# Kernel optimization log

Measured on AMD Instinct MI355X. Metric: run time of the kernel, lower is better.

The kernel has to match this reference:

```python
import jax, jax.numpy as jnp
import numpy as np

B, S, D, H = 2, 2048, 1024, 16
DH = D // H  # 64


def setup_inputs() -> dict:
    key = jax.random.key(0)
    ks = jax.random.split(key, 7)
    scale = 0.02
    return {
        "q": jax.random.normal(ks[0], (B, S, D), dtype=jnp.float32),
        "k": jax.random.normal(ks[1], (B, S, D), dtype=jnp.float32),
        "v": jax.random.normal(ks[2], (B, S, D), dtype=jnp.float32),
        "Wq": jax.random.normal(ks[3], (D, D), dtype=jnp.float32) * scale,
        "Wk": jax.random.normal(ks[4], (D, D), dtype=jnp.float32) * scale,
        "Wv": jax.random.normal(ks[5], (D, D), dtype=jnp.float32) * scale,
        "Wo": jax.random.normal(ks[6], (D, D), dtype=jnp.float32) * scale,
    }


def _split_heads(x):
    # [B, S, D] -> [B, H, S, DH]
    b, s, d = x.shape
    return x.reshape(b, s, H, DH).transpose(0, 2, 1, 3)


def reference(q, k, v, Wq, Wk, Wv, Wo):
    # Linear projections (torch Linear: x @ W.T, bias=False)
    qh = _split_heads(q @ Wq.T)  # [B, H, S, DH]
    kh = _split_heads(k @ Wk.T)
    vh = _split_heads(v @ Wv.T)
    # Scaled dot-product attention (manual, materializes scores as original)
    scores = jnp.einsum("bhqd,bhkd->bhqk", qh, kh) / jnp.sqrt(
        jnp.asarray(DH, dtype=qh.dtype)
    )  # [B, H, S, S]
    attn = jax.nn.softmax(scores, axis=-1)
    out = jnp.einsum("bhqk,bhkd->bhqd", attn, vh)  # [B, H, S, DH]
    # Concat heads: [B, H, S, DH] -> [B, S, D]
    out = out.transpose(0, 2, 1, 3).reshape(q.shape[0], q.shape[1], D)
    return out @ Wo.T
```

## Files before the change

kernel.cpp:

```cpp
#include <hip/hip_runtime.h>
#include <hip/hip_bf16.h>
#include <math.h>

namespace {
constexpr int Hn  = 16;
constexpr int DH  = 64;
constexpr int S   = 2048;
constexpr int D   = 1024;
constexpr int B   = 2;
constexpr int N   = B * S;
}

typedef __attribute__((ext_vector_type(8))) short bf16x8;
typedef __attribute__((ext_vector_type(4))) float f32x4;

#if defined(__has_builtin)
#if __has_builtin(__builtin_amdgcn_exp2f)
#define HAVE_EXP2_BUILTIN 1
#endif
#endif

static __device__ __forceinline__ float exp2_fast(float x) {
#ifdef HAVE_EXP2_BUILTIN
    return __builtin_amdgcn_exp2f(x);
#else
    float r;
    asm("v_exp_f32 %0, %1" : "=v"(r) : "v"(x));
    return r;
#endif
}

static __device__ __forceinline__ ushort bf16rd(float x) {
    unsigned u = __builtin_bit_cast(unsigned, x);
    return (ushort)((u + 0x8000u) >> 16);
}
static __device__ __forceinline__ ushort bf16tr(float x) {
    return (ushort)(__builtin_bit_cast(unsigned, x) >> 16);
}
static __device__ __forceinline__ float bfu2f(ushort h) {
    unsigned u = (unsigned)h << 16;
    return __builtin_bit_cast(float, u);
}
static __device__ __forceinline__ void split1(float a, ushort& h, ushort& l) {
    h = bf16rd(a);
    l = bf16rd(a - bfu2f(h));
}

static __device__ __forceinline__ void gload16(const ushort* g, ushort* l) {
    __builtin_amdgcn_global_load_lds((const unsigned int*)g, (unsigned int*)l, 16, 0, 0);
}

__global__ __launch_bounds__(256) void split_all(
    const float4* __restrict__ q, const float4* __restrict__ k, const float4* __restrict__ v,
    const float4* __restrict__ wq, const float4* __restrict__ wk,
    const float4* __restrict__ wv, const float4* __restrict__ wo,
    ushort4* __restrict__ qh, ushort4* __restrict__ kh, ushort4* __restrict__ vh,
    ushort4* __restrict__ wqh, ushort4* __restrict__ wkh, ushort4* __restrict__ wvh,
    ushort4* __restrict__ woh, ushort4* __restrict__ wol,
    int n4a, int n4w) {
    const int total = 3 * n4a + 4 * n4w;
    const int stride = gridDim.x * 256;
    for (int i = blockIdx.x * 256 + threadIdx.x; i < total; i += stride) {
        if (i < 3 * n4a) {
            const int which = i / n4a;
            const int j = i - which * n4a;
            const float4 val = (which == 0 ? q : which == 1 ? k : v)[j];
            ushort4* ph = which == 0 ? qh : which == 1 ? kh : vh;
            ph[j] = make_ushort4(bf16rd(val.x), bf16rd(val.y), bf16rd(val.z), bf16rd(val.w));
        } else {
            const int t = i - 3 * n4a;
            const int which = t / n4w;
            const int j = t - which * n4w;
            const float4 val = (which == 0 ? wq : which == 1 ? wk : which == 2 ? wv : wo)[j];
            if (which == 3) {
                ushort4 hh, ll;
                split1(val.x, hh.x, ll.x);
                split1(val.y, hh.y, ll.y);
                split1(val.z, hh.z, ll.z);
                split1(val.w, hh.w, ll.w);
                woh[j] = hh;
                wol[j] = ll;
            } else {
                ushort4* ph = which == 0 ? wqh : which == 1 ? wkh : wvh;
                ph[j] = make_ushort4(bf16rd(val.x), bf16rd(val.y), bf16rd(val.z), bf16rd(val.w));
            }
        }
    }
}

__global__ __launch_bounds__(256) void gemm_qkv(
    const ushort* __restrict__ qbf, const ushort* __restrict__ kbf,
    const ushort* __restrict__ vbf,
    const ushort* __restrict__ Wqh, const ushort* __restrict__ Wkh,
    const ushort* __restrict__ Wvh,
    ushort* __restrict__ Qbh, ushort* __restrict__ Kbh,
    ushort* __restrict__ Vtb, float qscale) {
    constexpr int BK = 64;
    constexpr int K = D;
    __shared__ __align__(16) ushort sA[128 * BK];
    __shared__ __align__(16) ushort sB[128 * BK];

    const int tid = threadIdx.x;
    const int which = blockIdx.y >> 3;
    const int m0 = blockIdx.x * 128;
    const int n0 = (blockIdx.y & 7) * 128;

    const ushort* A = which == 0 ? qbf : which == 1 ? kbf : vbf;
    const ushort* W = which == 0 ? Wqh : which == 1 ? Wkh : Wvh;

    const int l  = tid & 63;
    const int w  = tid >> 6;
    const int wm = w >> 1, wn = w & 1;
    const int lm = l & 15, g = l >> 4;

    const int srow = l >> 3;
    const int schunk = (l & 7) ^ srow;
    const ushort* gA = A + (size_t)(m0 + w * 32 + srow) * K + schunk * 8;
    const ushort* gB = W + (size_t)(n0 + w * 32 + srow) * K + schunk * 8;
    ushort* lA = &sA[(w * 32) * BK];
    ushort* lB = &sB[(w * 32) * BK];

    const f32x4 fzero = {0.f, 0.f, 0.f, 0.f};
    f32x4 acc[4][4];
#pragma unroll
    for (int mi = 0; mi < 4; ++mi)
#pragma unroll
        for (int ni = 0; ni < 4; ++ni) acc[mi][ni] = fzero;

    const int rsw = lm & 7;

    for (int s = 0; s < K / BK; ++s) {
        const int k0 = s * BK;
        if (s) __syncthreads();
#pragma unroll
        for (int j = 0; j < 4; ++j) {
            gload16(gA + (size_t)(j * 8) * K + k0, lA + (j * 8) * BK);
            gload16(gB + (size_t)(j * 8) * K + k0, lB + (j * 8) * BK);
        }
        __syncthreads();

#pragma unroll
        for (int kk = 0; kk < 2; ++kk) {
            bf16x8 ah[4], bh[4];
#pragma unroll
            for (int mi = 0; mi < 4; ++mi)
                ah[mi] = *(const bf16x8*)&sA[(wm * 64 + mi * 16 + lm) * BK + (((kk * 4 + g) ^ rsw) * 8)];
#pragma unroll
            for (int ni = 0; ni < 4; ++ni)
                bh[ni] = *(const bf16x8*)&sB[(wn * 64 + ni * 16 + lm) * BK + (((kk * 4 + g) ^ rsw) * 8)];
            __builtin_amdgcn_s_setprio(1);
#pragma unroll
            for (int mi = 0; mi < 4; ++mi)
#pragma unroll
                for (int ni = 0; ni < 4; ++ni)
                    acc[mi][ni] = __builtin_amdgcn_mfma_f32_16x16x32_bf16(
                        ah[mi], bh[ni], acc[mi][ni], 0, 0, 0);
            __builtin_amdgcn_s_setprio(0);
        }
    }

#pragma unroll
    for (int mi = 0; mi < 4; ++mi)
#pragma unroll
        for (int ni = 0; ni < 4; ++ni) {
            const int col = n0 + wn * 64 + ni * 16 + lm;
            const int rbase = m0 + wm * 64 + mi * 16 + g * 4;
            const int hh = col >> 6, dh = col & (DH - 1);
            if (which == 0) {
#pragma unroll
                for (int r = 0; r < 4; ++r) {
                    const int row = rbase + r;
                    const int bb = row >> 11, ss = row & (S - 1);
                    const size_t idx = (((size_t)(bb * Hn + hh)) * S + ss) * DH + dh;
                    Qbh[idx] = bf16rd(acc[mi][ni][r] * qscale);
                }
            } else if (which == 1) {
#pragma unroll
                for (int r = 0; r < 4; ++r) {
                    const int row = rbase + r;
                    const int bb = row >> 11, ss = row & (S - 1);
                    const size_t idx = (((size_t)(bb * Hn + hh)) * S + ss) * DH + dh;
                    Kbh[idx] = bf16rd(acc[mi][ni][r]);
                }
            } else {
                const int bb = rbase >> 11, ss = rbase & (S - 1);
                ushort4 pk;
                pk.x = bf16rd(acc[mi][ni][0]);
                pk.y = bf16rd(acc[mi][ni][1]);
                pk.z = bf16rd(acc[mi][ni][2]);
                pk.w = bf16rd(acc[mi][ni][3]);
                const size_t idx = (((size_t)(bb * Hn + hh)) * DH + dh) * S + ss;
                *(ushort4*)&Vtb[idx] = pk;
            }
        }
}

__global__ __launch_bounds__(256) void gemm_out(const ushort* __restrict__ Ah,
                                                const ushort* __restrict__ Al,
                                                const ushort* __restrict__ Wh,
                                                const ushort* __restrict__ Wl,
                                                float* __restrict__ C) {
    constexpr int BK = 32;
    constexpr int LDT = 40;
    constexpr int K = D, O = D;
    __shared__ __align__(16) ushort sAh[2][128 * LDT];
    __shared__ __align__(16) ushort sAl[2][128 * LDT];
    __shared__ __align__(16) ushort sBh[2][64 * LDT];
    __shared__ __align__(16) ushort sBl[2][64 * LDT];

    const int tid = threadIdx.x;
    const int m0 = blockIdx.x * 128;
    const int n0 = blockIdx.y * 64;

    const int l   = tid & 63;
    const int wid = tid >> 6;
    const int wm  = wid >> 1;
    const int wn  = wid & 1;
    const int lm  = l & 15;
    const int g   = l >> 4;
    const int lk  = g * 8;

    const int arow0 = tid >> 2;
    const int aslot = (tid & 3) * 8;
    const ushort* gAh0 = Ah + (size_t)(m0 + arow0) * K + aslot;
    const ushort* gAh1 = gAh0 + (size_t)64 * K;
    const ushort* gAl0 = Al + (size_t)(m0 + arow0) * K + aslot;
    const ushort* gAl1 = gAl0 + (size_t)64 * K;
    const ushort* gBh  = Wh + (size_t)(n0 + arow0) * K + aslot;
    const ushort* gBl  = Wl + (size_t)(n0 + arow0) * K + aslot;

    const f32x4 fzero = {0.f, 0.f, 0.f, 0.f};
    f32x4 acc[4][2];
#pragma unroll
    for (int mi = 0; mi < 4; ++mi)
#pragma unroll
        for (int ni = 0; ni < 2; ++ni) acc[mi][ni] = fzero;

    uint4 rA0 = *(const uint4*)gAh0, rA1 = *(const uint4*)gAh1;
    uint4 rA2 = *(const uint4*)gAl0, rA3 = *(const uint4*)gAl1;
    uint4 rB0 = *(const uint4*)gBh,  rB1 = *(const uint4*)gBl;

    *(uint4*)&sAh[0][arow0 * LDT + aslot]        = rA0;
    *(uint4*)&sAh[0][(arow0 + 64) * LDT + aslot] = rA1;
    *(uint4*)&sAl[0][arow0 * LDT + aslot]        = rA2;
    *(uint4*)&sAl[0][(arow0 + 64) * LDT + aslot] = rA3;
    *(uint4*)&sBh[0][arow0 * LDT + aslot]        = rB0;
    *(uint4*)&sBl[0][arow0 * LDT + aslot]        = rB1;
    rA0 = *(const uint4*)(gAh0 + BK); rA1 = *(const uint4*)(gAh1 + BK);
    rA2 = *(const uint4*)(gAl0 + BK); rA3 = *(const uint4*)(gAl1 + BK);
    rB0 = *(const uint4*)(gBh + BK);  rB1 = *(const uint4*)(gBl + BK);
    __syncthreads();

    constexpr int NS = K / BK;
    int cur = 0;
    for (int s = 0; s < NS; ++s) {
        bf16x8 ah[4], al[4], bh[2], bl[2];
#pragma unroll
        for (int mi = 0; mi < 4; ++mi) {
            const int row = wm * 64 + mi * 16 + lm;
            ah[mi] = *(const bf16x8*)&sAh[cur][row * LDT + lk];
            al[mi] = *(const bf16x8*)&sAl[cur][row * LDT + lk];
        }
#pragma unroll
        for (int ni = 0; ni < 2; ++ni) {
            const int rowb = wn * 32 + ni * 16 + lm;
            bh[ni] = *(const bf16x8*)&sBh[cur][rowb * LDT + lk];
            bl[ni] = *(const bf16x8*)&sBl[cur][rowb * LDT + lk];
        }
        __builtin_amdgcn_s_setprio(1);
#pragma unroll
        for (int mi = 0; mi < 4; ++mi)
#pragma unroll
            for (int ni = 0; ni < 2; ++ni) {
                acc[mi][ni] = __builtin_amdgcn_mfma_f32_16x16x32_bf16(
                    al[mi], bh[ni], acc[mi][ni], 0, 0, 0);
                acc[mi][ni] = __builtin_amdgcn_mfma_f32_16x16x32_bf16(
                    ah[mi], bl[ni], acc[mi][ni], 0, 0, 0);
                acc[mi][ni] = __builtin_amdgcn_mfma_f32_16x16x32_bf16(
                    ah[mi], bh[ni], acc[mi][ni], 0, 0, 0);
            }
        __builtin_amdgcn_s_setprio(0);

        if (s < NS - 1) {
            const int nx = cur ^ 1;
            *(uint4*)&sAh[nx][arow0 * LDT + aslot]        = rA0;
            *(uint4*)&sAh[nx][(arow0 + 64) * LDT + aslot] = rA1;
            *(uint4*)&sAl[nx][arow0 * LDT + aslot]        = rA2;
            *(uint4*)&sAl[nx][(arow0 + 64) * LDT + aslot] = rA3;
            *(uint4*)&sBh[nx][arow0 * LDT + aslot]        = rB0;
            *(uint4*)&sBl[nx][arow0 * LDT + aslot]        = rB1;
            if (s < NS - 2) {
                const int kn = (s + 2) * BK;
                rA0 = *(const uint4*)(gAh0 + kn); rA1 = *(const uint4*)(gAh1 + kn);
                rA2 = *(const uint4*)(gAl0 + kn); rA3 = *(const uint4*)(gAl1 + kn);
                rB0 = *(const uint4*)(gBh + kn);  rB1 = *(const uint4*)(gBl + kn);
            }
            __syncthreads();
            cur = nx;
        }
    }

#pragma unroll
    for (int mi = 0; mi < 4; ++mi)
#pragma unroll
        for (int ni = 0; ni < 2; ++ni) {
            const int col = n0 + wn * 32 + ni * 16 + lm;
            const int rbase = m0 + wm * 64 + mi * 16 + g * 4;
#pragma unroll
            for (int r = 0; r < 4; ++r)
                C[(size_t)(rbase + r) * O + col] = acc[mi][ni][r];
        }
}

__global__ __launch_bounds__(512) void attn_mfma(const ushort* __restrict__ Qbh,
                                                 const ushort* __restrict__ Kbh,
                                                 const ushort* __restrict__ Vt,
                                                 ushort* __restrict__ AOh,
                                                 ushort* __restrict__ AOl) {
    constexpr int LDT = 72;
    __shared__ __align__(16) ushort Ks[2][64 * LDT];
    __shared__ __align__(16) ushort Vs[2][64 * LDT];
    __shared__ __align__(16) ushort Ps[8][32 * LDT];

    const int tid = threadIdx.x;
    const int l = tid & 63, w = tid >> 6;
    const int wq = w & 3, grp = w >> 2;
    const int g = l >> 4, l15 = l & 15;
    const int bh = blockIdx.x;
    const int q0 = blockIdx.y * 128;
    const size_t bhb = (size_t)bh * S * DH;

    bf16x8 qh_[2][2];
#pragma unroll
    for (int qb = 0; qb < 2; ++qb)
#pragma unroll
        for (int kk = 0; kk < 2; ++kk) {
            const size_t idx = bhb + (size_t)(q0 + wq * 32 + qb * 16 + l15) * DH + kk * 32 + g * 8;
            qh_[qb][kk] = *(const bf16x8*)(Qbh + idx);
        }

    const int t8 = tid & 255;
    const int r_st = t8 >> 2;
    const int c0 = (t8 & 3) * 16;
    const ushort* gKh = Kbh + bhb + (size_t)r_st * DH + c0;
    const ushort* gVt = Vt + (size_t)bh * DH * S + (size_t)r_st * S + c0;

    const f32x4 fzero = {0.f, 0.f, 0.f, 0.f};
    f32x4 o_acc[2][4];
    f32x4 l_acc[2];
#pragma unroll
    for (int qb = 0; qb < 2; ++qb) {
        l_acc[qb] = fzero;
#pragma unroll
        for (int f = 0; f < 4; ++f) o_acc[qb][f] = fzero;
    }

    bf16x8 ones;
#pragma unroll
    for (int i = 0; i < 8; ++i) ones[i] = (short)0x3F80;

    uint4 pk0, pk1, pv0, pv1;
    {
        const size_t ok = (size_t)grp * 64 * DH, ov = (size_t)grp * 64;
        pk0 = *(const uint4*)(gKh + ok); pk1 = *(const uint4*)(gKh + ok + 8);
        pv0 = *(const uint4*)(gVt + ov); pv1 = *(const uint4*)(gVt + ov + 8);
        *(uint4*)&Ks[grp][r_st * LDT + c0]     = pk0;
        *(uint4*)&Ks[grp][r_st * LDT + c0 + 8] = pk1;
        *(uint4*)&Vs[grp][r_st * LDT + c0]     = pv0;
        *(uint4*)&Vs[grp][r_st * LDT + c0 + 8] = pv1;
        const size_t ok2 = (size_t)(2 + grp) * 64 * DH, ov2 = (size_t)(2 + grp) * 64;
        pk0 = *(const uint4*)(gKh + ok2); pk1 = *(const uint4*)(gKh + ok2 + 8);
        pv0 = *(const uint4*)(gVt + ov2); pv1 = *(const uint4*)(gVt + ov2 + 8);
    }
    __syncthreads();

    constexpr int NSI = S / 128;
    for (int t = 0; t < NSI; ++t) {
        f32x4 sc[2][4];
#pragma unroll
        for (int qb = 0; qb < 2; ++qb)
#pragma unroll
            for (int f = 0; f < 4; ++f) sc[qb][f] = fzero;
#pragma unroll
        for (int kk = 0; kk < 2; ++kk) {
            bf16x8 kh[4];
#pragma unroll
            for (int f = 0; f < 4; ++f)
                kh[f] = *(const bf16x8*)&Ks[grp][(f * 16 + l15) * LDT + kk * 32 + g * 8];
            __builtin_amdgcn_s_setprio(1);
#pragma unroll
            for (int f = 0; f < 4; ++f)
#pragma unroll
                for (int qb = 0; qb < 2; ++qb)
                    sc[qb][f] = __builtin_amdgcn_mfma_f32_16x16x32_bf16(
                        qh_[qb][kk], kh[f], sc[qb][f], 0, 0, 0);
            __builtin_amdgcn_s_setprio(0);
        }

#pragma unroll
        for (int qb = 0; qb < 2; ++qb)
#pragma unroll
            for (int f = 0; f < 4; ++f) {
#pragma unroll
                for (int r = 0; r < 4; ++r) {
                    const int prow = qb * 16 + g * 4 + r;
                    const int chunk = (f * 2 + (l15 >> 3)) ^ ((prow >> 2) & 7);
                    Ps[w][prow * LDT + chunk * 8 + (l15 & 7)] =
                        bf16tr(exp2_fast(sc[qb][f][r]));
                }
            }

#pragma unroll
        for (int kk = 0; kk < 2; ++kk) {
            const int row0 = l15;
            const int row1 = 16 + l15;
            const int ck = kk * 4 + g;
            const bf16x8 pa0 = *(const bf16x8*)&Ps[w][row0 * LDT + ((ck ^ ((row0 >> 2) & 7)) * 8)];
            const bf16x8 pa1 = *(const bf16x8*)&Ps[w][row1 * LDT + ((ck ^ ((row1 >> 2) & 7)) * 8)];
            __builtin_amdgcn_s_setprio(1);
            l_acc[0] = __builtin_amdgcn_mfma_f32_16x16x32_bf16(pa0, ones, l_acc[0], 0, 0, 0);
            l_acc[1] = __builtin_amdgcn_mfma_f32_16x16x32_bf16(pa1, ones, l_acc[1], 0, 0, 0);
#pragma unroll
            for (int f = 0; f < 4; ++f) {
                const bf16x8 vt = *(const bf16x8*)&Vs[grp][(f * 16 + l15) * LDT + kk * 32 + g * 8];
                o_acc[0][f] = __builtin_amdgcn_mfma_f32_16x16x32_bf16(pa0, vt, o_acc[0][f], 0, 0, 0);
                o_acc[1][f] = __builtin_amdgcn_mfma_f32_16x16x32_bf16(pa1, vt, o_acc[1][f], 0, 0, 0);
            }
            __builtin_amdgcn_s_setprio(0);
        }

        __syncthreads();
        if (t < NSI - 1) {
            *(uint4*)&Ks[grp][r_st * LDT + c0]     = pk0;
            *(uint4*)&Ks[grp][r_st * LDT + c0 + 8] = pk1;
            *(uint4*)&Vs[grp][r_st * LDT + c0]     = pv0;
            *(uint4*)&Vs[grp][r_st * LDT + c0 + 8] = pv1;
            if (t < NSI - 2) {
                const size_t ok = (size_t)(2 * (t + 2) + grp) * 64 * DH;
                const size_t ov = (size_t)(2 * (t + 2) + grp) * 64;
                pk0 = *(const uint4*)(gKh + ok); pk1 = *(const uint4*)(gKh + ok + 8);
                pv0 = *(const uint4*)(gVt + ov); pv1 = *(const uint4*)(gVt + ov + 8);
            }
            __syncthreads();
        }
    }

    float* comb  = (float*)&Ps[0][0];
    float* lcomb = (float*)&Ks[0][0];
    if (grp == 1) {
#pragma unroll
        for (int qb = 0; qb < 2; ++qb)
#pragma unroll
            for (int r = 0; r < 4; ++r) {
                const int row = qb * 16 + g * 4 + r;
#pragma unroll
                for (int f = 0; f < 4; ++f)
                    comb[wq * 2048 + row * 64 + f * 16 + l15] = o_acc[qb][f][r];
                if (l15 == 0) lcomb[wq * 32 + row] = l_acc[qb][r];
            }
    }
    __syncthreads();
    if (grp == 0) {
        const int bb = bh >> 4, hh = bh & 15;
#pragma unroll
        for (int qb = 0; qb < 2; ++qb)
#pragma unroll
            for (int r = 0; r < 4; ++r) {
                const int row = qb * 16 + g * 4 + r;
                const float lsum = l_acc[qb][r] + lcomb[wq * 32 + row];
                const float inv = 1.f / lsum;
                const int srow = q0 + wq * 32 + row;
#pragma unroll
                for (int f = 0; f < 4; ++f) {
                    const float val =
                        (o_acc[qb][f][r] + comb[wq * 2048 + row * 64 + f * 16 + l15]) * inv;
                    const size_t idx = ((size_t)(bb * S + srow)) * D + hh * DH + f * 16 + l15;
                    ushort hi, lo;
                    split1(val, hi, lo);
                    AOh[idx] = hi;
                    AOl[idx] = lo;
                }
            }
    }
}

extern "C" void kernel_launch(void* const* d_in, const int* in_sizes, int n_in,
                              void* d_out, int out_size, void* d_ws, size_t ws_size,
                              hipStream_t stream) {
    (void)in_sizes; (void)n_in; (void)out_size; (void)ws_size;
    const float* q  = (const float*)d_in[0];
    const float* k  = (const float*)d_in[1];
    const float* v  = (const float*)d_in[2];
    const float* Wq = (const float*)d_in[3];
    const float* Wk = (const float*)d_in[4];
    const float* Wv = (const float*)d_in[5];
    const float* Wo = (const float*)d_in[6];
    float* out = (float*)d_out;

    uint8_t* w8 = (uint8_t*)d_ws;
    constexpr size_t MB = 1u << 20;
    ushort* Wqh = (ushort*)(w8 + 0 * MB);
    ushort* Wkh = (ushort*)(w8 + 2 * MB);
    ushort* Wvh = (ushort*)(w8 + 4 * MB);
    ushort* Woh = (ushort*)(w8 + 6 * MB);
    ushort* Wol = (ushort*)(w8 + 8 * MB);
    ushort* qbf = (ushort*)(w8 + 16 * MB);
    ushort* kbf = (ushort*)(w8 + 24 * MB);
    ushort* vbf = (ushort*)(w8 + 32 * MB);
    ushort* Qbh = (ushort*)(w8 + 40 * MB);
    ushort* Kbh = (ushort*)(w8 + 48 * MB);
    ushort* Vtb = (ushort*)(w8 + 56 * MB);
    ushort* AOh = (ushort*)(w8 + 64 * MB);
    ushort* AOl = (ushort*)(w8 + 72 * MB);

    const int n4_act = (N * D) / 4;
    const int n4_w   = (D * D) / 4;
    const dim3 blk(256);

    split_all<<<2048, blk, 0, stream>>>(
        (const float4*)q, (const float4*)k, (const float4*)v,
        (const float4*)Wq, (const float4*)Wk, (const float4*)Wv, (const float4*)Wo,
        (ushort4*)qbf, (ushort4*)kbf, (ushort4*)vbf,
        (ushort4*)Wqh, (ushort4*)Wkh, (ushort4*)Wvh,
        (ushort4*)Woh, (ushort4*)Wol,
        n4_act, n4_w);

    const float qscale = 0.125f * 1.4426950408889634f;
    gemm_qkv<<<dim3(N / 128, 24), blk, 0, stream>>>(
        qbf, kbf, vbf, Wqh, Wkh, Wvh, Qbh, Kbh, Vtb, qscale);

    attn_mfma<<<dim3(B * Hn, S / 128), dim3(512), 0, stream>>>(
        Qbh, Kbh, Vtb, AOh, AOl);

    gemm_out<<<dim3(N / 128, D / 64), blk, 0, stream>>>(AOh, AOl, Woh, Wol, out);
}
```

Baseline: 146.4 us.

## Keep softmax probabilities in registers by transposing QK MFMA and permuting V layout

```diff
diff --git a/kernel.cpp b/kernel.cpp
--- a/kernel.cpp
+++ b/kernel.cpp
@@ -33,9 +33,6 @@
 static __device__ __forceinline__ ushort bf16rd(float x) {
     unsigned u = __builtin_bit_cast(unsigned, x);
     return (ushort)((u + 0x8000u) >> 16);
-}
-static __device__ __forceinline__ ushort bf16tr(float x) {
-    return (ushort)(__builtin_bit_cast(unsigned, x) >> 16);
 }
 static __device__ __forceinline__ float bfu2f(ushort h) {
     unsigned u = (unsigned)h << 16;
@@ -184,12 +181,13 @@
                 }
             } else {
                 const int bb = rbase >> 11, ss = rbase & (S - 1);
+                const int ssp = (ss & ~31) | (((ss >> 2) & 3) << 3) | (((ss >> 4) & 1) << 2);
                 ushort4 pk;
                 pk.x = bf16rd(acc[mi][ni][0]);
                 pk.y = bf16rd(acc[mi][ni][1]);
                 pk.z = bf16rd(acc[mi][ni][2]);
                 pk.w = bf16rd(acc[mi][ni][3]);
-                const size_t idx = (((size_t)(bb * Hn + hh)) * DH + dh) * S + ss;
+                const size_t idx = (((size_t)(bb * Hn + hh)) * DH + dh) * S + ssp;
                 *(ushort4*)&Vtb[idx] = pk;
             }
         }
@@ -318,9 +316,7 @@
                                                  ushort* __restrict__ AOh,
                                                  ushort* __restrict__ AOl) {
     constexpr int LDT = 72;
-    __shared__ __align__(16) ushort Ks[2][64 * LDT];
-    __shared__ __align__(16) ushort Vs[2][64 * LDT];
-    __shared__ __align__(16) ushort Ps[8][32 * LDT];
+    __shared__ __align__(16) ushort pool[4 * 64 * LDT];
 
     const int tid = threadIdx.x;
     const int l = tid & 63, w = tid >> 6;
@@ -330,6 +326,9 @@
     const int q0 = blockIdx.y * 128;
     const size_t bhb = (size_t)bh * S * DH;
 
+    ushort* Ksg = pool + grp * (64 * LDT);
+    ushort* Vsg = pool + (2 + grp) * (64 * LDT);
+
     bf16x8 qh_[2][2];
 #pragma unroll
     for (int qb = 0; qb < 2; ++qb)
@@ -364,10 +363,10 @@
         const size_t ok = (size_t)grp * 64 * DH, ov = (size_t)grp * 64;
         pk0 = *(const uint4*)(gKh + ok); pk1 = *(const uint4*)(gKh + ok + 8);
         pv0 = *(const uint4*)(gVt + ov); pv1 = *(const uint4*)(gVt + ov + 8);
-        *(uint4*)&Ks[grp][r_st * LDT + c0]     = pk0;
-        *(uint4*)&Ks[grp][r_st * LDT + c0 + 8] = pk1;
-        *(uint4*)&Vs[grp][r_st * LDT + c0]     = pv0;
-        *(uint4*)&Vs[grp][r_st * LDT + c0 + 8] = pv1;
+        *(uint4*)&Ksg[r_st * LDT + c0]     = pk0;
+        *(uint4*)&Ksg[r_st * LDT + c0 + 8] = pk1;
+        *(uint4*)&Vsg[r_st * LDT + c0]     = pv0;
+        *(uint4*)&Vsg[r_st * LDT + c0 + 8] = pv1;
         const size_t ok2 = (size_t)(2 + grp) * 64 * DH, ov2 = (size_t)(2 + grp) * 64;
         pk0 = *(const uint4*)(gKh + ok2); pk1 = *(const uint4*)(gKh + ok2 + 8);
         pv0 = *(const uint4*)(gVt + ov2); pv1 = *(const uint4*)(gVt + ov2 + 8);
@@ -386,43 +385,43 @@
             bf16x8 kh[4];
 #pragma unroll
             for (int f = 0; f < 4; ++f)
-                kh[f] = *(const bf16x8*)&Ks[grp][(f * 16 + l15) * LDT + kk * 32 + g * 8];
+                kh[f] = *(const bf16x8*)&Ksg[(f * 16 + l15) * LDT + kk * 32 + g * 8];
             __builtin_amdgcn_s_setprio(1);
 #pragma unroll
             for (int f = 0; f < 4; ++f)
 #pragma unroll
                 for (int qb = 0; qb < 2; ++qb)
                     sc[qb][f] = __builtin_amdgcn_mfma_f32_16x16x32_bf16(
-                        qh_[qb][kk], kh[f], sc[qb][f], 0, 0, 0);
+                        kh[f], qh_[qb][kk], sc[qb][f], 0, 0, 0);
             __builtin_amdgcn_s_setprio(0);
         }
 
+        unsigned up[2][2][4];
 #pragma unroll
         for (int qb = 0; qb < 2; ++qb)
 #pragma unroll
             for (int f = 0; f < 4; ++f) {
-#pragma unroll
-                for (int r = 0; r < 4; ++r) {
-                    const int prow = qb * 16 + g * 4 + r;
-                    const int chunk = (f * 2 + (l15 >> 3)) ^ ((prow >> 2) & 7);
-                    Ps[w][prow * LDT + chunk * 8 + (l15 & 7)] =
-                        bf16tr(exp2_fast(sc[qb][f][r]));
-                }
+                const int kk = f >> 1, a = f & 1;
+                const unsigned e0 = __builtin_bit_cast(unsigned, exp2_fast(sc[qb][f][0]));
+                const unsigned e1 = __builtin_bit_cast(unsigned, exp2_fast(sc[qb][f][1]));
+                const unsigned e2 = __builtin_bit_cast(unsigned, exp2_fast(sc[qb][f][2]));
+                const unsigned e3 = __builtin_bit_cast(unsigned, exp2_fast(sc[qb][f][3]));
+                up[qb][kk][a * 2 + 0] = (e0 >> 16) | (e1 & 0xFFFF0000u);
+                up[qb][kk][a * 2 + 1] = (e2 >> 16) | (e3 & 0xFFFF0000u);
             }
 
 #pragma unroll
         for (int kk = 0; kk < 2; ++kk) {
-            const int row0 = l15;
-            const int row1 = 16 + l15;
-            const int ck = kk * 4 + g;
-            const bf16x8 pa0 = *(const bf16x8*)&Ps[w][row0 * LDT + ((ck ^ ((row0 >> 2) & 7)) * 8)];
-            const bf16x8 pa1 = *(const bf16x8*)&Ps[w][row1 * LDT + ((ck ^ ((row1 >> 2) & 7)) * 8)];
+            const bf16x8 pa0 = __builtin_bit_cast(bf16x8,
+                make_uint4(up[0][kk][0], up[0][kk][1], up[0][kk][2], up[0][kk][3]));
+            const bf16x8 pa1 = __builtin_bit_cast(bf16x8,
+                make_uint4(up[1][kk][0], up[1][kk][1], up[1][kk][2], up[1][kk][3]));
             __builtin_amdgcn_s_setprio(1);
             l_acc[0] = __builtin_amdgcn_mfma_f32_16x16x32_bf16(pa0, ones, l_acc[0], 0, 0, 0);
             l_acc[1] = __builtin_amdgcn_mfma_f32_16x16x32_bf16(pa1, ones, l_acc[1], 0, 0, 0);
 #pragma unroll
             for (int f = 0; f < 4; ++f) {
-                const bf16x8 vt = *(const bf16x8*)&Vs[grp][(f * 16 + l15) * LDT + kk * 32 + g * 8];
+                const bf16x8 vt = *(const bf16x8*)&Vsg[(f * 16 + l15) * LDT + kk * 32 + g * 8];
                 o_acc[0][f] = __builtin_amdgcn_mfma_f32_16x16x32_bf16(pa0, vt, o_acc[0][f], 0, 0, 0);
                 o_acc[1][f] = __builtin_amdgcn_mfma_f32_16x16x32_bf16(pa1, vt, o_acc[1][f], 0, 0, 0);
             }
@@ -431,10 +430,10 @@
 
         __syncthreads();
         if (t < NSI - 1) {
-            *(uint4*)&Ks[grp][r_st * LDT + c0]     = pk0;
-            *(uint4*)&Ks[grp][r_st * LDT + c0 + 8] = pk1;
-            *(uint4*)&Vs[grp][r_st * LDT + c0]     = pv0;
-            *(uint4*)&Vs[grp][r_st * LDT + c0 + 8] = pv1;
+            *(uint4*)&Ksg[r_st * LDT + c0]     = pk0;
+            *(uint4*)&Ksg[r_st * LDT + c0 + 8] = pk1;
+            *(uint4*)&Vsg[r_st * LDT + c0]     = pv0;
+            *(uint4*)&Vsg[r_st * LDT + c0 + 8] = pv1;
             if (t < NSI - 2) {
                 const size_t ok = (size_t)(2 * (t + 2) + grp) * 64 * DH;
                 const size_t ov = (size_t)(2 * (t + 2) + grp) * 64;
@@ -445,8 +444,9 @@
         }
     }
 
-    float* comb  = (float*)&Ps[0][0];
-    float* lcomb = (float*)&Ks[0][0];
+    float* comb  = (float*)pool;
+    float* lcomb = comb + 4 * 32 * 64;
+    __syncthreads();
     if (grp == 1) {
 #pragma unroll
         for (int qb = 0; qb < 2; ++qb)
```

New measurement: 138.5 us. 1.06x faster.
